# Kernel tuning notes

Hardware: AMD Instinct MI355X
Metric: run time of the kernel (lower is better)

The kernel has to match this reference:

```python
import jax, jax.numpy as jnp
import numpy as np

# Dimensions: N sites, B batch, D bond dim, d physical dim, C output classes
N, B, D, d, C = 1024, 256, 16, 2, 10
STDDEV = 1e-5
INIT_DIAG = 1.0


def setup_inputs() -> dict:
    key = jax.random.key(0)
    k1, k2, k3 = jax.random.split(key, 3)
    x = jax.random.normal(k1, (N, B, d), dtype=jnp.float32)
    eye = jnp.eye(D, dtype=jnp.float32)
    # tensor[n,:,:,i] = init_diag * I + stddev * noise  (matches TF init)
    tensor = INIT_DIAG * eye[None, :, :, None] + STDDEV * jax.random.normal(k2, (N, D, D, d), dtype=jnp.float32)
    # Aout[c] = I + stddev * noise
    Aout = eye[None, :, :] + STDDEV * jax.random.normal(k3, (C, D, D), dtype=jnp.float32)
    return {"x": x, "tensor": tensor, "Aout": Aout}


def _chain_prod(A):
    # A: (n, b, D, D) -> ordered matrix-chain product (b, D, D), log-depth tree.
    # Faithful to parallel_contract: pairwise einsum per level; odd leftover is
    # kept at the end of the list (order-preserving, associativity-equivalent).
    while A.shape[0] > 1:
        n = A.shape[0]
        half = n // 2
        prod = jnp.einsum('nblk,nbkr->nblr', A[0:2 * half:2], A[1:2 * half:2])
        if n % 2 == 1:
            prod = jnp.concatenate([prod, A[-1:]], axis=0)
        A = prod
    return A[0]


def reference(x, tensor, Aout):
    # A: (N, B, D, D) site matrices after contracting input features
    A = jnp.einsum('nbi,nlri->nblr', x, tensor)
    nhalf = A.shape[0] // 2
    # Left half product, take row 0 (left boundary); right half, take col 0
    Al = _chain_prod(A[:nhalf])[:, 0, :]   # (B, D)
    Ar = _chain_prod(A[nhalf:])[:, :, 0]   # (B, D)
    # out[b,o] = Al[b] @ Aout[o] @ Ar[b]
    return jnp.einsum('bl,olr,br->bo', Al, Aout, Ar)
```

## Files before the change

### kernel.cpp

```cpp
#include <hip/hip_runtime.h>


#define BATCH  256
#define NCLS   10
#define NSITES 1024
#define NGRP   16
#define SEGLEN 16

typedef __attribute__((ext_vector_type(4))) float f32x4;
typedef __attribute__((ext_vector_type(4))) short short4b;
typedef __attribute__((ext_vector_type(2))) unsigned uint2v;
typedef __attribute__((ext_vector_type(4))) unsigned uint4v;
typedef __attribute__((ext_vector_type(4))) unsigned short us4;

static __device__ __forceinline__ unsigned short bf16tr(float f) {
    return (unsigned short)(__builtin_bit_cast(unsigned, f) >> 16);
}
static __device__ __forceinline__ unsigned short bf16rne(float f) {
    unsigned u = __builtin_bit_cast(unsigned, f);
    u += 0x7FFFu + ((u >> 16) & 1u);
    return (unsigned short)(u >> 16);
}
static __device__ __forceinline__ float bf16tof(unsigned short h) {
    return __builtin_bit_cast(float, (unsigned)h << 16);
}
static __device__ __forceinline__ unsigned fbits(float f) {
    return __builtin_bit_cast(unsigned, f);
}
static __device__ __forceinline__ float lo16(unsigned u) {
    return __builtin_bit_cast(float, u << 16);
}
static __device__ __forceinline__ float hi16(unsigned u) {
    return __builtin_bit_cast(float, u & 0xffff0000u);
}
static __device__ __forceinline__ unsigned pkhi(float hi, float lo) {
    return __builtin_amdgcn_perm(fbits(hi), fbits(lo), 0x07060302u);
}
static __device__ __forceinline__ short4b mk4(unsigned lo, unsigned hi) {
    uint2v u; u.x = lo; u.y = hi;
    return __builtin_bit_cast(short4b, u);
}
static __device__ __forceinline__ f32x4 mfma16(short4b a, short4b b, f32x4 c) {
#if __has_builtin(__builtin_amdgcn_mfma_f32_16x16x16bf16_1k)
    return __builtin_amdgcn_mfma_f32_16x16x16bf16_1k(a, b, c, 0, 0, 0);
#else
    f32x4 d;
    asm volatile("v_mfma_f32_16x16x16_bf16 %0, %1, %2, %3"
                 : "=v"(d) : "v"(a), "v"(b), "v"(c));
    return d;
#endif
}

__global__ __launch_bounds__(256) void ta_pack_kernel(
    const float* __restrict__ tensor, unsigned short* __restrict__ Ta)
{
    __shared__ float s[512];
    const int n = blockIdx.x, t = threadIdx.x;
    *(float2*)(s + 2 * t) = *(const float2*)(tensor + (size_t)n * 512 + 2 * t);
    __syncthreads();
    const int o0 = 2 * t;
    const int lane = o0 >> 3, e0 = o0 & 7;
    const int q = lane >> 4, m = lane & 15;
    const int i = e0 >> 2, j0 = e0 & 3;
    const int k0 = 4 * q + j0;
    const float v0 = s[k0 * 32 + m * 2 + i];
    const float v1 = s[(k0 + 1) * 32 + m * 2 + i];
    ((unsigned*)Ta)[(size_t)n * 256 + t] =
        (unsigned)bf16rne(v0) | ((unsigned)bf16rne(v1) << 16);
}

__global__ __launch_bounds__(256) void chain_kernel(
    const float* __restrict__ x,
    const unsigned short* __restrict__ Ta,
    unsigned short* __restrict__ M2)
{
    __shared__ __align__(16) unsigned short rm[4 * 256];
    __shared__ __align__(16) unsigned short cm[4 * 256];
    const int t = threadIdx.x, wave = t >> 6, lane = t & 63;
    const int quad = lane >> 4, l15 = lane & 15;
    const int b = blockIdx.x & 255, g = blockIdx.x >> 8;
    const int seg = g * 4 + wave, n0 = seg * SEGLEN;

    f32x4 d;
#pragma unroll
    for (int r = 0; r < 4; ++r) d[r] = (quad * 4 + r == l15) ? 1.0f : 0.0f;

    const float2* __restrict__ xp = (const float2*)x;
    const uint4v* __restrict__ tp = (const uint4v*)Ta + (size_t)n0 * 64 + lane;

#pragma unroll 4
    for (int s = 0; s < SEGLEN; ++s) {
        const int n = n0 + s;
        const float2 xv = xp[(size_t)n * BATCH + b];
        const uint4v tw = tp[(size_t)s * 64];
        const float a0 = __builtin_fmaf(xv.x, lo16(tw.x), xv.y * lo16(tw.z));
        const float a1 = __builtin_fmaf(xv.x, hi16(tw.x), xv.y * hi16(tw.z));
        const float a2 = __builtin_fmaf(xv.x, lo16(tw.y), xv.y * lo16(tw.w));
        const float a3 = __builtin_fmaf(xv.x, hi16(tw.y), xv.y * hi16(tw.w));
        const short4b af = mk4(pkhi(a1, a0), pkhi(a3, a2));
        const short4b bf = mk4(pkhi(d[1], d[0]), pkhi(d[3], d[2]));
        f32x4 c0 = {0.0f, 0.0f, 0.0f, 0.0f};
        d = mfma16(af, bf, c0);
    }

#pragma unroll
    for (int r = 0; r < 4; ++r)
        rm[wave * 256 + (quad * 4 + r) * 16 + l15] = bf16tr(d[r]);
    {
        us4 pk = {bf16tr(d[0]), bf16tr(d[1]), bf16tr(d[2]), bf16tr(d[3])};
        *(us4*)(cm + wave * 256 + l15 * 16 + quad * 4) = pk;
    }
    __syncthreads();

    short4b af1 = {0, 0, 0, 0}, bf1 = {0, 0, 0, 0};
    if (wave < 2) {
        af1 = __builtin_bit_cast(short4b,
              *(const uint2v*)(rm + (2 * wave + 1) * 256 + l15 * 16 + quad * 4));
        bf1 = __builtin_bit_cast(short4b,
              *(const uint2v*)(cm + (2 * wave) * 256 + l15 * 16 + quad * 4));
    }
    __syncthreads();
    if (wave < 2) {
        f32x4 c0 = {0.0f, 0.0f, 0.0f, 0.0f};
        f32x4 q = mfma16(af1, bf1, c0);
#pragma unroll
        for (int r = 0; r < 4; ++r)
            rm[wave * 256 + (quad * 4 + r) * 16 + l15] = bf16tr(q[r]);
        us4 pk = {bf16tr(q[0]), bf16tr(q[1]), bf16tr(q[2]), bf16tr(q[3])};
        *(us4*)(cm + wave * 256 + l15 * 16 + quad * 4) = pk;
    }
    __syncthreads();

    if (wave == 0) {
        const short4b af2 = __builtin_bit_cast(short4b,
              *(const uint2v*)(rm + 1 * 256 + l15 * 16 + quad * 4));
        const short4b bf2 = __builtin_bit_cast(short4b,
              *(const uint2v*)(cm + 0 * 256 + l15 * 16 + quad * 4));
        f32x4 c0 = {0.0f, 0.0f, 0.0f, 0.0f};
        f32x4 rr = mfma16(af2, bf2, c0);
        us4 pk = {bf16tr(rr[0]), bf16tr(rr[1]), bf16tr(rr[2]), bf16tr(rr[3])};
        *(us4*)(M2 + ((size_t)b * NGRP + g) * 256 + l15 * 16 + quad * 4) = pk;
    }
}

__global__ __launch_bounds__(256) void combine_kernel(
    const unsigned short* __restrict__ M2,
    const float* __restrict__ Aout,
    float* __restrict__ out)
{
    __shared__ __align__(16) unsigned short rm[16 * 256];
    __shared__ __align__(16) unsigned short cm[16 * 256];
    const int b = blockIdx.x, t = threadIdx.x;
    const int wave = t >> 6, lane = t & 63, quad = lane >> 4, l15 = lane & 15;
    typedef __attribute__((ext_vector_type(8))) short short8;

    const short8* __restrict__ src = (const short8*)(M2 + (size_t)b * NGRP * 256);
#pragma unroll
    for (int i2 = 0; i2 < 2; ++i2) {
        const int i = t + 256 * i2;
        const short8 v = src[i];
        *((short8*)cm + i) = v;
        const int mat = i >> 5, c = (i >> 1) & 15, r0 = (i & 1) * 8;
#pragma unroll
        for (int e = 0; e < 8; ++e)
            rm[mat * 256 + (r0 + e) * 16 + c] = (unsigned short)v[e];
    }
    __syncthreads();

    for (int lvl = 0; lvl < 3; ++lvl) {
        const int np = 8 >> lvl;
        short4b afr[2], bfr[2];
        int pids[2], nmine = 0;
        for (int p = wave; p < np; p += 4) {
            afr[nmine] = __builtin_bit_cast(short4b,
                 *(const uint2v*)(rm + (2 * p + 1) * 256 + l15 * 16 + quad * 4));
            bfr[nmine] = __builtin_bit_cast(short4b,
                 *(const uint2v*)(cm + (2 * p) * 256 + l15 * 16 + quad * 4));
            pids[nmine] = p; ++nmine;
        }
        __syncthreads();
        for (int ii = 0; ii < nmine; ++ii) {
            f32x4 c0 = {0.0f, 0.0f, 0.0f, 0.0f};
            f32x4 r = mfma16(afr[ii], bfr[ii], c0);
            const int p = pids[ii];
#pragma unroll
            for (int rr = 0; rr < 4; ++rr)
                rm[p * 256 + (quad * 4 + rr) * 16 + l15] = bf16tr(r[rr]);
            us4 pk = {bf16tr(r[0]), bf16tr(r[1]), bf16tr(r[2]), bf16tr(r[3])};
            *(us4*)(cm + p * 256 + l15 * 16 + quad * 4) = pk;
        }
        __syncthreads();
    }

    if (t < NCLS * 16) {
        const int o = t >> 4, r = t & 15;
        const float vr = bf16tof(rm[256 + r]);
        float s = 0.0f;
#pragma unroll
        for (int l = 0; l < 16; ++l)
            s = __builtin_fmaf(bf16tof(rm[l * 16]), Aout[((size_t)o * 16 + l) * 16 + r], s);
        s *= vr;
#pragma unroll
        for (int off = 8; off > 0; off >>= 1)
            s += __shfl_xor(s, off, 16);
        if (r == 0) out[(size_t)b * NCLS + o] = s;
    }
}

extern "C" void kernel_launch(void* const* d_in, const int* in_sizes, int n_in,
                              void* d_out, int out_size, void* d_ws, size_t ws_size,
                              hipStream_t stream)
{
    const float* x      = (const float*)d_in[0];
    const float* tensor = (const float*)d_in[1];
    const float* Aout   = (const float*)d_in[2];
    float* out = (float*)d_out;

    unsigned short* Ta = (unsigned short*)d_ws;
    unsigned short* M2 = (unsigned short*)((char*)d_ws + (1 << 20));

    ta_pack_kernel<<<NSITES, 256, 0, stream>>>(tensor, Ta);
    chain_kernel<<<BATCH * NGRP, 256, 0, stream>>>(x, Ta, M2);
    combine_kernel<<<BATCH, 256, 0, stream>>>(M2, Aout, out);
}
```

Before: 81.53 us.

## Batch eight samples per chain block to reuse site tensors and interleave MFMA chains

Each chain_kernel block now processes 8 batch elements instead of 1. Every loaded site-tensor fragment is reused across all 8 chains, and the 8 independent dependent-MFMA chains are interleaved to hide MFMA latency. The tree reduction in shared memory is reorganised so all four waves stay busy. The grid shrinks from 4096 to 512 blocks, and per-thread registers and shared memory grow, which could reduce occupancy.

```diff
diff --git a/kernel.cpp b/kernel.cpp
--- a/kernel.cpp
+++ b/kernel.cpp
@@ -6,6 +6,7 @@
 #define NSITES 1024
 #define NGRP   16
 #define SEGLEN 16
+#define NB     8
 
 typedef __attribute__((ext_vector_type(4))) float f32x4;
 typedef __attribute__((ext_vector_type(4))) short short4b;
@@ -74,72 +75,101 @@
     const unsigned short* __restrict__ Ta,
     unsigned short* __restrict__ M2)
 {
-    __shared__ __align__(16) unsigned short rm[4 * 256];
-    __shared__ __align__(16) unsigned short cm[4 * 256];
+    __shared__ __align__(16) unsigned short rm[32 * 256];
+    __shared__ __align__(16) unsigned short cm[32 * 256];
     const int t = threadIdx.x, wave = t >> 6, lane = t & 63;
     const int quad = lane >> 4, l15 = lane & 15;
-    const int b = blockIdx.x & 255, g = blockIdx.x >> 8;
+    const int bt = blockIdx.x & 31, g = blockIdx.x >> 5;
+    const int b0 = bt * NB;
     const int seg = g * 4 + wave, n0 = seg * SEGLEN;
 
-    f32x4 d;
-#pragma unroll
-    for (int r = 0; r < 4; ++r) d[r] = (quad * 4 + r == l15) ? 1.0f : 0.0f;
-
-    const float2* __restrict__ xp = (const float2*)x;
+    f32x4 d[NB];
+#pragma unroll
+    for (int j = 0; j < NB; ++j)
+#pragma unroll
+        for (int r = 0; r < 4; ++r) d[j][r] = (quad * 4 + r == l15) ? 1.0f : 0.0f;
+
     const uint4v* __restrict__ tp = (const uint4v*)Ta + (size_t)n0 * 64 + lane;
 
 #pragma unroll 4
     for (int s = 0; s < SEGLEN; ++s) {
         const int n = n0 + s;
-        const float2 xv = xp[(size_t)n * BATCH + b];
         const uint4v tw = tp[(size_t)s * 64];
-        const float a0 = __builtin_fmaf(xv.x, lo16(tw.x), xv.y * lo16(tw.z));
-        const float a1 = __builtin_fmaf(xv.x, hi16(tw.x), xv.y * hi16(tw.z));
-        const float a2 = __builtin_fmaf(xv.x, lo16(tw.y), xv.y * lo16(tw.w));
-        const float a3 = __builtin_fmaf(xv.x, hi16(tw.y), xv.y * hi16(tw.w));
-        const short4b af = mk4(pkhi(a1, a0), pkhi(a3, a2));
-        const short4b bf = mk4(pkhi(d[1], d[0]), pkhi(d[3], d[2]));
+        const float2* __restrict__ xv = (const float2*)(x + ((size_t)n * BATCH + b0) * 2);
+        float2 xs[NB];
+#pragma unroll
+        for (int j = 0; j < NB; ++j) xs[j] = xv[j];
+        const float t00 = lo16(tw.x), t01 = hi16(tw.x), t02 = lo16(tw.y), t03 = hi16(tw.y);
+        const float t10 = lo16(tw.z), t11 = hi16(tw.z), t12 = lo16(tw.w), t13 = hi16(tw.w);
+#pragma unroll
+        for (int j = 0; j < NB; ++j) {
+            const float a0 = __builtin_fmaf(xs[j].x, t00, xs[j].y * t10);
+            const float a1 = __builtin_fmaf(xs[j].x, t01, xs[j].y * t11);
+            const float a2 = __builtin_fmaf(xs[j].x, t02, xs[j].y * t12);
+            const float a3 = __builtin_fmaf(xs[j].x, t03, xs[j].y * t13);
+            const short4b af = mk4(pkhi(a1, a0), pkhi(a3, a2));
+            const short4b bf = mk4(pkhi(d[j][1], d[j][0]), pkhi(d[j][3], d[j][2]));
+            f32x4 c0 = {0.0f, 0.0f, 0.0f, 0.0f};
+            d[j] = mfma16(af, bf, c0);
+        }
+    }
+
+    if (wave & 1) {
+#pragma unroll
+        for (int j = 0; j < NB; ++j) {
+            const int sl = j * 4 + wave;
+#pragma unroll
+            for (int r = 0; r < 4; ++r)
+                rm[sl * 256 + (quad * 4 + r) * 16 + l15] = bf16tr(d[j][r]);
+        }
+    } else {
+#pragma unroll
+        for (int j = 0; j < NB; ++j) {
+            const int sl = j * 4 + wave;
+            us4 pk = {bf16tr(d[j][0]), bf16tr(d[j][1]), bf16tr(d[j][2]), bf16tr(d[j][3])};
+            *(us4*)(cm + sl * 256 + l15 * 16 + quad * 4) = pk;
+        }
+    }
+    __syncthreads();
+
+    short4b af1[4], bf1[4];
+#pragma unroll
+    for (int i = 0; i < 4; ++i) {
+        const int p = 4 * wave + i, j = p >> 1, h = p & 1;
+        af1[i] = __builtin_bit_cast(short4b,
+            *(const uint2v*)(rm + (j * 4 + 2 * h + 1) * 256 + l15 * 16 + quad * 4));
+        bf1[i] = __builtin_bit_cast(short4b,
+            *(const uint2v*)(cm + (j * 4 + 2 * h) * 256 + l15 * 16 + quad * 4));
+    }
+    __syncthreads();
+#pragma unroll
+    for (int i = 0; i < 4; ++i) {
+        const int p = 4 * wave + i, j = p >> 1, h = p & 1;
         f32x4 c0 = {0.0f, 0.0f, 0.0f, 0.0f};
-        d = mfma16(af, bf, c0);
-    }
-
-#pragma unroll
-    for (int r = 0; r < 4; ++r)
-        rm[wave * 256 + (quad * 4 + r) * 16 + l15] = bf16tr(d[r]);
-    {
-        us4 pk = {bf16tr(d[0]), bf16tr(d[1]), bf16tr(d[2]), bf16tr(d[3])};
-        *(us4*)(cm + wave * 256 + l15 * 16 + quad * 4) = pk;
-    }
-    __syncthreads();
-
-    short4b af1 = {0, 0, 0, 0}, bf1 = {0, 0, 0, 0};
-    if (wave < 2) {
-        af1 = __builtin_bit_cast(short4b,
-              *(const uint2v*)(rm + (2 * wave + 1) * 256 + l15 * 16 + quad * 4));
-        bf1 = __builtin_bit_cast(short4b,
-              *(const uint2v*)(cm + (2 * wave) * 256 + l15 * 16 + quad * 4));
-    }
-    __syncthreads();
-    if (wave < 2) {
-        f32x4 c0 = {0.0f, 0.0f, 0.0f, 0.0f};
-        f32x4 q = mfma16(af1, bf1, c0);
-#pragma unroll
-        for (int r = 0; r < 4; ++r)
-            rm[wave * 256 + (quad * 4 + r) * 16 + l15] = bf16tr(q[r]);
-        us4 pk = {bf16tr(q[0]), bf16tr(q[1]), bf16tr(q[2]), bf16tr(q[3])};
-        *(us4*)(cm + wave * 256 + l15 * 16 + quad * 4) = pk;
-    }
-    __syncthreads();
-
-    if (wave == 0) {
+        f32x4 q = mfma16(af1[i], bf1[i], c0);
+        const int sl = j * 4 + h;
+        if (h) {
+#pragma unroll
+            for (int r = 0; r < 4; ++r)
+                rm[sl * 256 + (quad * 4 + r) * 16 + l15] = bf16tr(q[r]);
+        } else {
+            us4 pk = {bf16tr(q[0]), bf16tr(q[1]), bf16tr(q[2]), bf16tr(q[3])};
+            *(us4*)(cm + sl * 256 + l15 * 16 + quad * 4) = pk;
+        }
+    }
+    __syncthreads();
+
+#pragma unroll
+    for (int i = 0; i < 2; ++i) {
+        const int j = 2 * wave + i;
         const short4b af2 = __builtin_bit_cast(short4b,
-              *(const uint2v*)(rm + 1 * 256 + l15 * 16 + quad * 4));
+            *(const uint2v*)(rm + (j * 4 + 1) * 256 + l15 * 16 + quad * 4));
         const short4b bf2 = __builtin_bit_cast(short4b,
-              *(const uint2v*)(cm + 0 * 256 + l15 * 16 + quad * 4));
+            *(const uint2v*)(cm + (j * 4 + 0) * 256 + l15 * 16 + quad * 4));
         f32x4 c0 = {0.0f, 0.0f, 0.0f, 0.0f};
         f32x4 rr = mfma16(af2, bf2, c0);
         us4 pk = {bf16tr(rr[0]), bf16tr(rr[1]), bf16tr(rr[2]), bf16tr(rr[3])};
-        *(us4*)(M2 + ((size_t)b * NGRP + g) * 256 + l15 * 16 + quad * 4) = pk;
+        *(us4*)(M2 + ((size_t)(b0 + j) * NGRP + g) * 256 + l15 * 16 + quad * 4) = pk;
     }
 }
 
@@ -220,6 +250,6 @@
     unsigned short* M2 = (unsigned short*)((char*)d_ws + (1 << 20));
 
     ta_pack_kernel<<<NSITES, 256, 0, stream>>>(tensor, Ta);
-    chain_kernel<<<BATCH * NGRP, 256, 0, stream>>>(x, Ta, M2);
+    chain_kernel<<<BATCH * NGRP / NB, 256, 0, stream>>>(x, Ta, M2);
     combine_kernel<<<BATCH, 256, 0, stream>>>(M2, Aout, out);
 }
```

Measured after the change: 77.14 us. 5.4% less time.
